# Kernel tuning notes

Measured on AMD Instinct MI355X. Metric: run time of the kernel, lower is better.

## Reference

```python
import jax, jax.numpy as jnp
import numpy as np

LN_EPS = 1e-5

def setup_inputs() -> dict:
    key = jax.random.key(0)
    ks = jax.random.split(key, 10)
    N, E, H, V, L, OUT, G = 100000, 600000, 128, 65, 4, 32, 64
    x_tokens = jax.random.randint(ks[0], (N, 2), 0, V, dtype=jnp.int32)
    edge_index = jax.random.randint(ks[1], (2, E), 0, N, dtype=jnp.int32)
    batch = jnp.sort(jax.random.randint(ks[2], (N,), 0, G)).astype(jnp.int64)
    s = 0.05
    key_emb = jax.random.normal(ks[3], (V, H), jnp.float32) * s
    val_emb = jax.random.normal(ks[4], (V, H), jnp.float32) * s
    Ws = jax.random.normal(ks[5], (L, H, H), jnp.float32) * (1.0 / np.sqrt(H))
    bs = jax.random.normal(ks[6], (L, H), jnp.float32) * s
    ln_g = jnp.ones((L, H), jnp.float32)
    ln_b = jnp.zeros((L, H), jnp.float32)
    out_W = jax.random.normal(ks[7], (OUT, H), jnp.float32) * (1.0 / np.sqrt(H))
    return {"x_tokens": x_tokens, "edge_index": edge_index, "batch": batch,
            "key_emb": key_emb, "val_emb": val_emb, "Ws": Ws, "bs": bs,
            "ln_g": ln_g, "ln_b": ln_b, "out_W": out_W}

def _layer_norm(x, g, b):
    mu = jnp.mean(x, axis=-1, keepdims=True)
    var = jnp.mean(jnp.square(x - mu), axis=-1, keepdims=True)
    return (x - mu) * jax.lax.rsqrt(var + LN_EPS) * g + b

def reference(x_tokens, edge_index, batch, key_emb, val_emb, Ws, bs, ln_g, ln_b, out_W):
    N = x_tokens.shape[0]
    L = Ws.shape[0]
    # layer-0: key + value embedding lookup -> [N, H]
    x = key_emb[x_tokens[:, 0]] + val_emb[x_tokens[:, 1]]
    # GCN normalization with self-loops (computed once; edges fixed per layer)
    loop = jnp.arange(N, dtype=edge_index.dtype)
    src = jnp.concatenate([edge_index[0], loop])  # [E+N]
    dst = jnp.concatenate([edge_index[1], loop])
    deg = jax.ops.segment_sum(jnp.ones_like(dst, dtype=x.dtype), dst, num_segments=N)
    dis = jnp.where(deg > 0, jax.lax.rsqrt(jnp.maximum(deg, 1.0)), 0.0)
    norm = (dis[src] * dis[dst])[:, None]  # [E+N, 1]
    for i in range(L):
        xw = x @ Ws[i]  # [N, H]
        agg = jax.ops.segment_sum(norm * xw[src], dst, num_segments=N) + bs[i]
        new_x = jax.nn.relu(agg)          # use_activation
        x = x + new_x                      # use_residual
        x = _layer_norm(x, ln_g[i], ln_b[i])  # use_layer_norm
    logits = x @ out_W.T  # Linear(bias=False) -> [N, out_dim]
    return logits
```

## Files before the change

### kernel.cpp

```cpp
#include <hip/hip_runtime.h>

#define H 128
#define LN_EPS 1e-5f
#define TROW 66

typedef unsigned short u16;
typedef unsigned int u32;
typedef __attribute__((ext_vector_type(8))) short bf16x8;
typedef __attribute__((ext_vector_type(4))) float f32x4;

__device__ __forceinline__ float bflo(u32 u){ return __uint_as_float(u << 16); }
__device__ __forceinline__ float bfhi(u32 u){ return __uint_as_float(u & 0xFFFF0000u); }
__device__ __forceinline__ float bf1(u16 u){ return __uint_as_float(((u32)u) << 16); }
__device__ __forceinline__ u16 f2bu(float f){
  u32 u = __float_as_uint(f);
  return (u16)((u + 0x7FFFu + ((u >> 16) & 1u)) >> 16);
}

__device__ __forceinline__ float ldf(const void* p, int i, bool isbf){
  return isbf ? bf1(reinterpret_cast<const u16*>(p)[i])
              : reinterpret_cast<const float*>(p)[i];
}


__global__ void k_convert(const void* __restrict__ kemb, const void* __restrict__ vemb,
                          const void* __restrict__ Ws,   const void* __restrict__ bs,
                          const void* __restrict__ lng,  const void* __restrict__ lnb,
                          const void* __restrict__ outW,
                          float* __restrict__ kemb_f, float* __restrict__ vemb_f,
                          u16* __restrict__ W_c, float* __restrict__ bs_f,
                          float* __restrict__ lng_f, float* __restrict__ lnb_f,
                          u16* __restrict__ outW_b, int* __restrict__ flag,
                          int V, int L, int OUT){
  bool isbf = (*reinterpret_cast<const u32*>(lng) == 0x3F803F80u);
  if (blockIdx.x == 0 && threadIdx.x == 0) flag[0] = isbf ? 1 : 0;
  int i = blockIdx.x * blockDim.x + threadIdx.x;
  int nEmb = V * H;
  int nW   = L * H * H;
  int nVec = L * H;
  int nOut = OUT * H;
  if (i < nEmb){ kemb_f[i] = ldf(kemb, i, isbf); vemb_f[i] = ldf(vemb, i, isbf); }
  if (i < nW){
    int j = i & 7, lane = (i >> 3) & 63, g = i >> 9;
    int s = g & 3, cg = (g >> 2) & 7, l = g >> 5;
    int k = s * 32 + (lane >> 4) * 8 + j;
    int n = cg * 16 + (lane & 15);
    W_c[i] = f2bu(ldf(Ws, l * H * H + k * H + n, isbf));
  }
  if (i < nVec){ bs_f[i] = ldf(bs, i, isbf); lng_f[i] = ldf(lng, i, isbf);
                 lnb_f[i] = ldf(lnb, i, isbf); }
  if (i < nOut){ outW_b[i] = f2bu(ldf(outW, i, isbf)); }
}


__global__ void k_count(const int* __restrict__ dst, int E, int* __restrict__ deg){
  int i = blockIdx.x * blockDim.x + threadIdx.x;
  if (i < E) atomicAdd(&deg[dst[i]], 1);
}

__device__ __forceinline__ int paddedLen(int d){ return (d + 4) & ~3; }

__global__ void k_bsum(const int* __restrict__ deg, int* __restrict__ bsum, int N){
  __shared__ int sh[256];
  int i = blockIdx.x * 256 + threadIdx.x;
  sh[threadIdx.x] = (i < N) ? paddedLen(deg[i]) : 0;
  __syncthreads();
  for (int off = 128; off > 0; off >>= 1){
    if (threadIdx.x < off) sh[threadIdx.x] += sh[threadIdx.x + off];
    __syncthreads();
  }
  if (threadIdx.x == 0) bsum[blockIdx.x] = sh[0];
}

__global__ void k_bscan(int* __restrict__ bsum, int nb){
  __shared__ int sh[1024];
  int t = threadIdx.x;
  sh[t] = (t < nb) ? bsum[t] : 0;
  __syncthreads();
  for (int off = 1; off < 1024; off <<= 1){
    int add = (t >= off) ? sh[t - off] : 0;
    __syncthreads();
    sh[t] += add;
    __syncthreads();
  }
  if (t < nb) bsum[t] = (t > 0) ? sh[t - 1] : 0;
}

__global__ void k_scan2(const int* __restrict__ deg, const int* __restrict__ bsum,
                        int* __restrict__ row_ptr, float* __restrict__ dis,
                        int* __restrict__ cursor, int2* __restrict__ csr, int N){
  __shared__ int sh[256];
  int i = blockIdx.x * 256 + threadIdx.x;
  int d = (i < N) ? deg[i] : 0;
  int v = (i < N) ? paddedLen(d) : 0;
  sh[threadIdx.x] = v;
  __syncthreads();
  for (int off = 1; off < 256; off <<= 1){
    int add = (threadIdx.x >= off) ? sh[threadIdx.x - off] : 0;
    __syncthreads();
    sh[threadIdx.x] += add;
    __syncthreads();
  }
  int excl = sh[threadIdx.x] - v + bsum[blockIdx.x];
  if (i < N){
    row_ptr[i] = excl;
    float r = rsqrtf((float)(d + 1));
    dis[i] = r;
    cursor[i] = 1;
    csr[excl] = make_int2(i * (H / 2), __float_as_int(r * r));
    for (int p = excl + d + 1; p < excl + v; p++)
      csr[p] = make_int2(0, 0);
  }
  if (i == N - 1) row_ptr[N] = excl + v;
}

__global__ void k_fill(const int* __restrict__ src, const int* __restrict__ dst, int E,
                       const float* __restrict__ dis, const int* __restrict__ row_ptr,
                       int* __restrict__ cursor, int2* __restrict__ csr){
  int i = blockIdx.x * blockDim.x + threadIdx.x;
  if (i >= E) return;
  int s = src[i], d = dst[i];
  int pos = atomicAdd(&cursor[d], 1);
  csr[row_ptr[d] + pos] = make_int2(s * (H / 2), __float_as_int(dis[s] * dis[d]));
}


__global__ __launch_bounds__(256) void k_embed(const int* __restrict__ tok,
                        const float* __restrict__ kemb, const float* __restrict__ vemb,
                        u16* __restrict__ xb, int N){
  int n = blockIdx.x * 4 + (threadIdx.x >> 6);
  if (n >= N) return;
  int h0 = (threadIdx.x & 63) * 2;
  int t0 = tok[n * 2], t1 = tok[n * 2 + 1];
  float2 k2 = *reinterpret_cast<const float2*>(&kemb[t0 * H + h0]);
  float2 v2 = *reinterpret_cast<const float2*>(&vemb[t1 * H + h0]);
  *reinterpret_cast<u32*>(&xb[(size_t)n * H + h0]) =
      (u32)f2bu(k2.x + v2.x) | ((u32)f2bu(k2.y + v2.y) << 16);
}


__global__ __launch_bounds__(256) void k_gemm(const u16* __restrict__ xb,
                                              const u16* __restrict__ Wc,
                                              u16* __restrict__ xw, int npairs){
  int wid = threadIdx.x >> 6, lane = threadIdx.x & 63;
  int sp = wid >> 1;
  int ch = wid & 1;
  int r = lane & 15, kq = lane >> 4;
  bf16x8 wf[4][4];
  #pragma unroll
  for (int c = 0; c < 4; c++)
    #pragma unroll
    for (int s = 0; s < 4; s++)
      wf[c][s] = *reinterpret_cast<const bf16x8*>(
          Wc + (size_t)((((ch * 4 + c) * 4 + s) * 64 + lane) << 3));
  for (int p = blockIdx.x; p < npairs; p += gridDim.x){
    int node0 = (p * 2 + sp) << 4;
    const u16* xrow = xb + (size_t)node0 * H + r * H + kq * 8;
    bf16x8 xf[4];
    #pragma unroll
    for (int s = 0; s < 4; s++)
      xf[s] = *reinterpret_cast<const bf16x8*>(xrow + s * 32);
    f32x4 acc[4] = {{0,0,0,0},{0,0,0,0},{0,0,0,0},{0,0,0,0}};
    #pragma unroll
    for (int s = 0; s < 4; s++)
      #pragma unroll
      for (int c = 0; c < 4; c++)
        acc[c] = __builtin_amdgcn_mfma_f32_16x16x32_bf16(wf[c][s], xf[s], acc[c], 0, 0, 0);
    u16* orow = xw + (size_t)(node0 + r) * H + ch * 64 + kq * 4;
    #pragma unroll
    for (int c = 0; c < 4; c++){
      u32 lo = (u32)f2bu(acc[c][0]) | ((u32)f2bu(acc[c][1]) << 16);
      u32 hi = (u32)f2bu(acc[c][2]) | ((u32)f2bu(acc[c][3]) << 16);
      *reinterpret_cast<uint2*>(orow + c * 16) = make_uint2(lo, hi);
    }
  }
}


__device__ __forceinline__ void gather2(const u32* __restrict__ xw32,
    const int* __restrict__ row_ptr, const int2* __restrict__ csr,
    const float* __restrict__ bias, const float* __restrict__ gamma,
    const float* __restrict__ beta,
    u16* __restrict__ xb, int N, u32* __restrict__ tile, bool writeGlobal){
  int lane = threadIdx.x & 63;
  int w = threadIdx.x >> 6;
  int n0 = blockIdx.x * 16 + 2 * w;
  int h0 = lane * 2;
  if (n0 >= N){
    tile[(2 * w) * TROW + lane] = 0;
    tile[(2 * w + 1) * TROW + lane] = 0;
    return;
  }
  bool two = (n0 + 1 < N);
  const int4* csr4 = reinterpret_cast<const int4*>(csr);
  int rs0 = __builtin_amdgcn_readfirstlane(row_ptr[n0]);
  int rm  = __builtin_amdgcn_readfirstlane(row_ptr[n0 + 1]);
  int re1 = two ? __builtin_amdgcn_readfirstlane(row_ptr[n0 + 2]) : rm;
  int len0 = rm - rs0, len1 = re1 - rm;
  int common = min(len0, len1);
  u32 xv0 = *reinterpret_cast<const u32*>(&xb[(size_t)n0 * H + h0]);
  u32 xv1 = two ? *reinterpret_cast<const u32*>(&xb[(size_t)(n0 + 1) * H + h0]) : 0u;
  float2 b2 = *reinterpret_cast<const float2*>(&bias[h0]);
  float2 g2 = *reinterpret_cast<const float2*>(&gamma[h0]);
  float2 t2 = *reinterpret_cast<const float2*>(&beta[h0]);
  float a00 = 0.f, a01 = 0.f, a10 = 0.f, a11 = 0.f;
#define EDGE(CX, CY, A0, A1) { \
    u32 cx = (u32)__builtin_amdgcn_readfirstlane(CX); \
    float wgt = __uint_as_float((u32)__builtin_amdgcn_readfirstlane(CY)); \
    u32 v = xw32[cx + lane]; \
    A0 = fmaf(wgt, bflo(v), A0); A1 = fmaf(wgt, bfhi(v), A1); }
  int i = 0;
  for (; i < common; i += 4){
    int4 ca = csr4[(rs0 + i) >> 1], cb = csr4[((rs0 + i) >> 1) + 1];
    int4 da = csr4[(rm + i) >> 1],  db = csr4[((rm + i) >> 1) + 1];
    EDGE(ca.x, ca.y, a00, a01) EDGE(da.x, da.y, a10, a11)
    EDGE(ca.z, ca.w, a00, a01) EDGE(da.z, da.w, a10, a11)
    EDGE(cb.x, cb.y, a00, a01) EDGE(db.x, db.y, a10, a11)
    EDGE(cb.z, cb.w, a00, a01) EDGE(db.z, db.w, a10, a11)
  }
  for (; i < len0; i += 4){
    int4 ca = csr4[(rs0 + i) >> 1], cb = csr4[((rs0 + i) >> 1) + 1];
    EDGE(ca.x, ca.y, a00, a01) EDGE(ca.z, ca.w, a00, a01)
    EDGE(cb.x, cb.y, a00, a01) EDGE(cb.z, cb.w, a00, a01)
  }
  for (; i < len1; i += 4){
    int4 da = csr4[(rm + i) >> 1], db = csr4[((rm + i) >> 1) + 1];
    EDGE(da.x, da.y, a10, a11) EDGE(da.z, da.w, a10, a11)
    EDGE(db.x, db.y, a10, a11) EDGE(db.z, db.w, a10, a11)
  }
#undef EDGE
  float v0 = fmaxf(a00 + b2.x, 0.f), v1 = fmaxf(a01 + b2.y, 0.f);
  v0 += bflo(xv0); v1 += bfhi(xv0);
  float u0 = fmaxf(a10 + b2.x, 0.f), u1 = fmaxf(a11 + b2.y, 0.f);
  u0 += bflo(xv1); u1 += bfhi(xv1);
  float s0 = v0 + v1, s1 = u0 + u1;
  #pragma unroll
  for (int off = 32; off > 0; off >>= 1){
    s0 += __shfl_xor(s0, off);
    s1 += __shfl_xor(s1, off);
  }
  float mu0 = s0 * (1.f / 128.f), mu1 = s1 * (1.f / 128.f);
  float d00 = v0 - mu0, d01 = v1 - mu0;
  float d10 = u0 - mu1, d11 = u1 - mu1;
  float q0 = d00 * d00 + d01 * d01, q1 = d10 * d10 + d11 * d11;
  #pragma unroll
  for (int off = 32; off > 0; off >>= 1){
    q0 += __shfl_xor(q0, off);
    q1 += __shfl_xor(q1, off);
  }
  float inv0 = rsqrtf(q0 * (1.f / 128.f) + LN_EPS);
  float inv1 = rsqrtf(q1 * (1.f / 128.f) + LN_EPS);
  u32 w0 = (u32)f2bu(d00 * inv0 * g2.x + t2.x) |
           ((u32)f2bu(d01 * inv0 * g2.y + t2.y) << 16);
  u32 w1 = (u32)f2bu(d10 * inv1 * g2.x + t2.x) |
           ((u32)f2bu(d11 * inv1 * g2.y + t2.y) << 16);
  tile[(2 * w) * TROW + lane] = w0;
  tile[(2 * w + 1) * TROW + lane] = two ? w1 : 0u;
  if (writeGlobal){
    *reinterpret_cast<u32*>(&xb[(size_t)n0 * H + h0]) = w0;
    if (two)
      *reinterpret_cast<u32*>(&xb[(size_t)(n0 + 1) * H + h0]) = w1;
  }
}

__global__ __launch_bounds__(512) void k_fgemm(const u32* __restrict__ xw32,
    const int* __restrict__ row_ptr, const int2* __restrict__ csr,
    const float* __restrict__ bias, const float* __restrict__ gamma,
    const float* __restrict__ beta,
    u16* __restrict__ xb, const u16* __restrict__ Wc,
    u16* __restrict__ xw_out, int N){
  __shared__ u32 tile[16 * TROW];
  int lane = threadIdx.x & 63, w = threadIdx.x >> 6;
  int r = lane & 15, kq = lane >> 4;
  bf16x8 wfr[4];
  #pragma unroll
  for (int s = 0; s < 4; s++)
    wfr[s] = *reinterpret_cast<const bf16x8*>(Wc + (size_t)(((w * 4 + s) * 64 + lane) << 3));
  gather2(xw32, row_ptr, csr, bias, gamma, beta, xb, N, tile, true);
  __syncthreads();
  int node = blockIdx.x * 16 + r;
  if (node >= N) return;
  const u16* t16 = reinterpret_cast<const u16*>(tile);
  f32x4 acc = {0.f, 0.f, 0.f, 0.f};
  #pragma unroll
  for (int s = 0; s < 4; s++){
    bf16x8 xf = *reinterpret_cast<const bf16x8*>(t16 + r * (2 * TROW) + s * 32 + kq * 8);
    acc = __builtin_amdgcn_mfma_f32_16x16x32_bf16(wfr[s], xf, acc, 0, 0, 0);
  }
  u32 lo = (u32)f2bu(acc[0]) | ((u32)f2bu(acc[1]) << 16);
  u32 hi = (u32)f2bu(acc[2]) | ((u32)f2bu(acc[3]) << 16);
  *reinterpret_cast<uint2*>(xw_out + (size_t)node * H + w * 16 + kq * 4) =
      make_uint2(lo, hi);
}

__global__ __launch_bounds__(512) void k_fout(const u32* __restrict__ xw32,
    const int* __restrict__ row_ptr, const int2* __restrict__ csr,
    const float* __restrict__ bias, const float* __restrict__ gamma,
    const float* __restrict__ beta,
    u16* __restrict__ xb, const u16* __restrict__ oWb,
    u16* __restrict__ out16, float* __restrict__ outf,
    const int* __restrict__ flag, int N){
  __shared__ u32 tile[16 * TROW];
  int lane = threadIdx.x & 63, w = threadIdx.x >> 6;
  int r = lane & 15, kq = lane >> 4;
  bf16x8 wfr[4];
  if (w < 2){
    #pragma unroll
    for (int s = 0; s < 4; s++)
      wfr[s] = *reinterpret_cast<const bf16x8*>(oWb + (w * 16 + r) * H + s * 32 + kq * 8);
  }
  gather2(xw32, row_ptr, csr, bias, gamma, beta, xb, N, tile, false);
  __syncthreads();
  if (w >= 2) return;
  int node = blockIdx.x * 16 + r;
  if (node >= N) return;
  const u16* t16 = reinterpret_cast<const u16*>(tile);
  f32x4 acc = {0.f, 0.f, 0.f, 0.f};
  #pragma unroll
  for (int s = 0; s < 4; s++){
    bf16x8 xf = *reinterpret_cast<const bf16x8*>(t16 + r * (2 * TROW) + s * 32 + kq * 8);
    acc = __builtin_amdgcn_mfma_f32_16x16x32_bf16(wfr[s], xf, acc, 0, 0, 0);
  }
  if (flag[0]){
    u32 lo = (u32)f2bu(acc[0]) | ((u32)f2bu(acc[1]) << 16);
    u32 hi = (u32)f2bu(acc[2]) | ((u32)f2bu(acc[3]) << 16);
    *reinterpret_cast<uint2*>(out16 + (size_t)node * 32 + w * 16 + kq * 4) =
        make_uint2(lo, hi);
  } else {
    *reinterpret_cast<f32x4*>(outf + (size_t)node * 32 + w * 16 + kq * 4) = acc;
  }
}


extern "C" void kernel_launch(void* const* d_in, const int* in_sizes, int n_in,
                              void* d_out, int out_size, void* d_ws, size_t ws_size,
                              hipStream_t stream){
  const int*  x_tokens = (const int*)d_in[0];
  const int*  edge_idx = (const int*)d_in[1];
  const void* kemb = d_in[3];
  const void* vemb = d_in[4];
  const void* Ws   = d_in[5];
  const void* bs   = d_in[6];
  const void* lng  = d_in[7];
  const void* lnb  = d_in[8];
  const void* outW = d_in[9];

  int N   = in_sizes[0] / 2;
  int E   = in_sizes[1] / 2;
  int V   = in_sizes[3] / H;
  int L   = in_sizes[5] / (H * H);
  int OUT = in_sizes[9] / H;

  char* ws = (char*)d_ws;
  size_t off = 0;
  auto alloc = [&](size_t bytes) -> void* {
    void* p = ws + off;
    off += (bytes + 255) & ~(size_t)255;
    return p;
  };
  u16*   xb     = (u16*)  alloc((size_t)N * H * 2);
  u16*   xwA    = (u16*)  alloc((size_t)N * H * 2);
  u16*   xwB    = (u16*)  alloc((size_t)N * H * 2);
  int*   deg    = (int*)  alloc((size_t)N * 4);
  int*   cursor = (int*)  alloc((size_t)N * 4);
  int*   row_ptr= (int*)  alloc((size_t)(N + 1) * 4);
  float* dis    = (float*)alloc((size_t)N * 4);
  int*   bsum   = (int*)  alloc(1024 * 4);
  int2*  csr    = (int2*) alloc(((size_t)E + 4 * (size_t)N) * 8);
  float* kemb_f = (float*)alloc((size_t)V * H * 4);
  float* vemb_f = (float*)alloc((size_t)V * H * 4);
  u16*   W_c    = (u16*)  alloc((size_t)L * H * H * 2);
  float* bs_f   = (float*)alloc((size_t)L * H * 4);
  float* lng_f  = (float*)alloc((size_t)L * H * 4);
  float* lnb_f  = (float*)alloc((size_t)L * H * 4);
  u16*   outW_b = (u16*)  alloc((size_t)OUT * H * 2);
  int*   flag   = (int*)  alloc(256);

  const int* esrc = edge_idx;
  const int* edst = edge_idx + E;

  (void)hipMemsetAsync(deg, 0, (size_t)N * 4, stream);

  int convTotal = L * H * H;
  int cb = (convTotal + 255) / 256;
  k_convert<<<cb, 256, 0, stream>>>(kemb, vemb, Ws, bs, lng, lnb, outW,
                                    kemb_f, vemb_f, W_c, bs_f, lng_f, lnb_f,
                                    outW_b, flag, V, L, OUT);

  int eb = (E + 255) / 256;
  int nb = (N + 255) / 256;
  k_count<<<eb, 256, 0, stream>>>(edst, E, deg);
  k_bsum <<<nb, 256, 0, stream>>>(deg, bsum, N);
  k_bscan<<<1, 1024, 0, stream>>>(bsum, nb);
  k_scan2<<<nb, 256, 0, stream>>>(deg, bsum, row_ptr, dis, cursor, csr, N);
  k_fill <<<eb, 256, 0, stream>>>(esrc, edst, E, dis, row_ptr, cursor, csr);
  k_embed<<<(N + 3) / 4, 256, 0, stream>>>(x_tokens, kemb_f, vemb_f, xb, N);

  int nstrips = (N + 15) / 16;
  int npairs  = (nstrips + 1) / 2;
  k_gemm<<<1024, 256, 0, stream>>>(xb, W_c, xwA, npairs);
  u16* xw_in = xwA; u16* xw_out = xwB;
  for (int l = 0; l < L - 1; l++){
    k_fgemm<<<nstrips, 512, 0, stream>>>((const u32*)xw_in, row_ptr, csr,
                                         bs_f + l * H, lng_f + l * H, lnb_f + l * H,
                                         xb, W_c + (size_t)(l + 1) * H * H,
                                         xw_out, N);
    u16* t = xw_in; xw_in = xw_out; xw_out = t;
  }
  k_fout<<<nstrips, 512, 0, stream>>>((const u32*)xw_in, row_ptr, csr,
                                      bs_f + (L - 1) * H, lng_f + (L - 1) * H,
                                      lnb_f + (L - 1) * H,
                                      xb, outW_b, (u16*)d_out, (float*)d_out,
                                      flag, N);
}
```

Baseline: 297.2 us.

## Gather four nodes per wavefront and halve block size in fused layers

```diff
diff --git a/kernel.cpp b/kernel.cpp
--- a/kernel.cpp
+++ b/kernel.cpp
@@ -177,93 +177,136 @@
 }
 
 
-__device__ __forceinline__ void gather2(const u32* __restrict__ xw32,
+__device__ __forceinline__ void gather4(const u32* __restrict__ xw32,
     const int* __restrict__ row_ptr, const int2* __restrict__ csr,
     const float* __restrict__ bias, const float* __restrict__ gamma,
     const float* __restrict__ beta,
     u16* __restrict__ xb, int N, u32* __restrict__ tile, bool writeGlobal){
   int lane = threadIdx.x & 63;
   int w = threadIdx.x >> 6;
-  int n0 = blockIdx.x * 16 + 2 * w;
+  int n0 = blockIdx.x * 16 + 4 * w;
   int h0 = lane * 2;
-  if (n0 >= N){
-    tile[(2 * w) * TROW + lane] = 0;
-    tile[(2 * w + 1) * TROW + lane] = 0;
-    return;
-  }
-  bool two = (n0 + 1 < N);
   const int4* csr4 = reinterpret_cast<const int4*>(csr);
-  int rs0 = __builtin_amdgcn_readfirstlane(row_ptr[n0]);
-  int rm  = __builtin_amdgcn_readfirstlane(row_ptr[n0 + 1]);
-  int re1 = two ? __builtin_amdgcn_readfirstlane(row_ptr[n0 + 2]) : rm;
-  int len0 = rm - rs0, len1 = re1 - rm;
-  int common = min(len0, len1);
-  u32 xv0 = *reinterpret_cast<const u32*>(&xb[(size_t)n0 * H + h0]);
-  u32 xv1 = two ? *reinterpret_cast<const u32*>(&xb[(size_t)(n0 + 1) * H + h0]) : 0u;
+  int rp0 = __builtin_amdgcn_readfirstlane(row_ptr[min(n0, N)]);
+  int rp1 = __builtin_amdgcn_readfirstlane(row_ptr[min(n0 + 1, N)]);
+  int rp2 = __builtin_amdgcn_readfirstlane(row_ptr[min(n0 + 2, N)]);
+  int rp3 = __builtin_amdgcn_readfirstlane(row_ptr[min(n0 + 3, N)]);
+  int rp4 = __builtin_amdgcn_readfirstlane(row_ptr[min(n0 + 4, N)]);
+  int l0 = rp1 - rp0, l1 = rp2 - rp1, l2 = rp3 - rp2, l3 = rp4 - rp3;
+  bool val0 = n0 < N, val1 = n0 + 1 < N, val2 = n0 + 2 < N, val3 = n0 + 3 < N;
+  u32 xv0 = val0 ? *reinterpret_cast<const u32*>(&xb[(size_t)n0 * H + h0]) : 0u;
+  u32 xv1 = val1 ? *reinterpret_cast<const u32*>(&xb[(size_t)(n0 + 1) * H + h0]) : 0u;
+  u32 xv2 = val2 ? *reinterpret_cast<const u32*>(&xb[(size_t)(n0 + 2) * H + h0]) : 0u;
+  u32 xv3 = val3 ? *reinterpret_cast<const u32*>(&xb[(size_t)(n0 + 3) * H + h0]) : 0u;
   float2 b2 = *reinterpret_cast<const float2*>(&bias[h0]);
   float2 g2 = *reinterpret_cast<const float2*>(&gamma[h0]);
   float2 t2 = *reinterpret_cast<const float2*>(&beta[h0]);
   float a00 = 0.f, a01 = 0.f, a10 = 0.f, a11 = 0.f;
+  float a20 = 0.f, a21 = 0.f, a30 = 0.f, a31 = 0.f;
 #define EDGE(CX, CY, A0, A1) { \
     u32 cx = (u32)__builtin_amdgcn_readfirstlane(CX); \
     float wgt = __uint_as_float((u32)__builtin_amdgcn_readfirstlane(CY)); \
     u32 v = xw32[cx + lane]; \
     A0 = fmaf(wgt, bflo(v), A0); A1 = fmaf(wgt, bfhi(v), A1); }
+  int c01 = min(l0, l1), c23 = min(l2, l3), c4 = min(c01, c23);
   int i = 0;
-  for (; i < common; i += 4){
-    int4 ca = csr4[(rs0 + i) >> 1], cb = csr4[((rs0 + i) >> 1) + 1];
-    int4 da = csr4[(rm + i) >> 1],  db = csr4[((rm + i) >> 1) + 1];
-    EDGE(ca.x, ca.y, a00, a01) EDGE(da.x, da.y, a10, a11)
-    EDGE(ca.z, ca.w, a00, a01) EDGE(da.z, da.w, a10, a11)
-    EDGE(cb.x, cb.y, a00, a01) EDGE(db.x, db.y, a10, a11)
-    EDGE(cb.z, cb.w, a00, a01) EDGE(db.z, db.w, a10, a11)
-  }
-  for (; i < len0; i += 4){
-    int4 ca = csr4[(rs0 + i) >> 1], cb = csr4[((rs0 + i) >> 1) + 1];
-    EDGE(ca.x, ca.y, a00, a01) EDGE(ca.z, ca.w, a00, a01)
-    EDGE(cb.x, cb.y, a00, a01) EDGE(cb.z, cb.w, a00, a01)
-  }
-  for (; i < len1; i += 4){
-    int4 da = csr4[(rm + i) >> 1], db = csr4[((rm + i) >> 1) + 1];
-    EDGE(da.x, da.y, a10, a11) EDGE(da.z, da.w, a10, a11)
-    EDGE(db.x, db.y, a10, a11) EDGE(db.z, db.w, a10, a11)
+  for (; i < c4; i += 4){
+    int4 A0 = csr4[(rp0 + i) >> 1], B0 = csr4[((rp0 + i) >> 1) + 1];
+    int4 A1 = csr4[(rp1 + i) >> 1], B1 = csr4[((rp1 + i) >> 1) + 1];
+    int4 A2 = csr4[(rp2 + i) >> 1], B2 = csr4[((rp2 + i) >> 1) + 1];
+    int4 A3 = csr4[(rp3 + i) >> 1], B3 = csr4[((rp3 + i) >> 1) + 1];
+    EDGE(A0.x, A0.y, a00, a01) EDGE(A1.x, A1.y, a10, a11)
+    EDGE(A2.x, A2.y, a20, a21) EDGE(A3.x, A3.y, a30, a31)
+    EDGE(A0.z, A0.w, a00, a01) EDGE(A1.z, A1.w, a10, a11)
+    EDGE(A2.z, A2.w, a20, a21) EDGE(A3.z, A3.w, a30, a31)
+    EDGE(B0.x, B0.y, a00, a01) EDGE(B1.x, B1.y, a10, a11)
+    EDGE(B2.x, B2.y, a20, a21) EDGE(B3.x, B3.y, a30, a31)
+    EDGE(B0.z, B0.w, a00, a01) EDGE(B1.z, B1.w, a10, a11)
+    EDGE(B2.z, B2.w, a20, a21) EDGE(B3.z, B3.w, a30, a31)
+  }
+  int j = i;
+  for (; j < c01; j += 4){
+    int4 A0 = csr4[(rp0 + j) >> 1], B0 = csr4[((rp0 + j) >> 1) + 1];
+    int4 A1 = csr4[(rp1 + j) >> 1], B1 = csr4[((rp1 + j) >> 1) + 1];
+    EDGE(A0.x, A0.y, a00, a01) EDGE(A1.x, A1.y, a10, a11)
+    EDGE(A0.z, A0.w, a00, a01) EDGE(A1.z, A1.w, a10, a11)
+    EDGE(B0.x, B0.y, a00, a01) EDGE(B1.x, B1.y, a10, a11)
+    EDGE(B0.z, B0.w, a00, a01) EDGE(B1.z, B1.w, a10, a11)
+  }
+  int j0 = j;
+  for (; j0 < l0; j0 += 4){
+    int4 A0 = csr4[(rp0 + j0) >> 1], B0 = csr4[((rp0 + j0) >> 1) + 1];
+    EDGE(A0.x, A0.y, a00, a01) EDGE(A0.z, A0.w, a00, a01)
+    EDGE(B0.x, B0.y, a00, a01) EDGE(B0.z, B0.w, a00, a01)
+  }
+  int j1 = j;
+  for (; j1 < l1; j1 += 4){
+    int4 A1 = csr4[(rp1 + j1) >> 1], B1 = csr4[((rp1 + j1) >> 1) + 1];
+    EDGE(A1.x, A1.y, a10, a11) EDGE(A1.z, A1.w, a10, a11)
+    EDGE(B1.x, B1.y, a10, a11) EDGE(B1.z, B1.w, a10, a11)
+  }
+  int k = i;
+  for (; k < c23; k += 4){
+    int4 A2 = csr4[(rp2 + k) >> 1], B2 = csr4[((rp2 + k) >> 1) + 1];
+    int4 A3 = csr4[(rp3 + k) >> 1], B3 = csr4[((rp3 + k) >> 1) + 1];
+    EDGE(A2.x, A2.y, a20, a21) EDGE(A3.x, A3.y, a30, a31)
+    EDGE(A2.z, A2.w, a20, a21) EDGE(A3.z, A3.w, a30, a31)
+    EDGE(B2.x, B2.y, a20, a21) EDGE(B3.x, B3.y, a30, a31)
+    EDGE(B2.z, B2.w, a20, a21) EDGE(B3.z, B3.w, a30, a31)
+  }
+  int k2 = k;
+  for (; k2 < l2; k2 += 4){
+    int4 A2 = csr4[(rp2 + k2) >> 1], B2 = csr4[((rp2 + k2) >> 1) + 1];
+    EDGE(A2.x, A2.y, a20, a21) EDGE(A2.z, A2.w, a20, a21)
+    EDGE(B2.x, B2.y, a20, a21) EDGE(B2.z, B2.w, a20, a21)
+  }
+  int k3 = k;
+  for (; k3 < l3; k3 += 4){
+    int4 A3 = csr4[(rp3 + k3) >> 1], B3 = csr4[((rp3 + k3) >> 1) + 1];
+    EDGE(A3.x, A3.y, a30, a31) EDGE(A3.z, A3.w, a30, a31)
+    EDGE(B3.x, B3.y, a30, a31) EDGE(B3.z, B3.w, a30, a31)
   }
 #undef EDGE
-  float v0 = fmaxf(a00 + b2.x, 0.f), v1 = fmaxf(a01 + b2.y, 0.f);
-  v0 += bflo(xv0); v1 += bfhi(xv0);
-  float u0 = fmaxf(a10 + b2.x, 0.f), u1 = fmaxf(a11 + b2.y, 0.f);
-  u0 += bflo(xv1); u1 += bfhi(xv1);
-  float s0 = v0 + v1, s1 = u0 + u1;
+  float v0 = fmaxf(a00 + b2.x, 0.f) + bflo(xv0), v1 = fmaxf(a01 + b2.y, 0.f) + bfhi(xv0);
+  float u0 = fmaxf(a10 + b2.x, 0.f) + bflo(xv1), u1 = fmaxf(a11 + b2.y, 0.f) + bfhi(xv1);
+  float p0 = fmaxf(a20 + b2.x, 0.f) + bflo(xv2), p1 = fmaxf(a21 + b2.y, 0.f) + bfhi(xv2);
+  float r0 = fmaxf(a30 + b2.x, 0.f) + bflo(xv3), r1 = fmaxf(a31 + b2.y, 0.f) + bfhi(xv3);
+  float s0 = v0 + v1, s1 = u0 + u1, s2 = p0 + p1, s3 = r0 + r1;
   #pragma unroll
   for (int off = 32; off > 0; off >>= 1){
-    s0 += __shfl_xor(s0, off);
-    s1 += __shfl_xor(s1, off);
+    s0 += __shfl_xor(s0, off); s1 += __shfl_xor(s1, off);
+    s2 += __shfl_xor(s2, off); s3 += __shfl_xor(s3, off);
   }
   float mu0 = s0 * (1.f / 128.f), mu1 = s1 * (1.f / 128.f);
-  float d00 = v0 - mu0, d01 = v1 - mu0;
-  float d10 = u0 - mu1, d11 = u1 - mu1;
+  float mu2 = s2 * (1.f / 128.f), mu3 = s3 * (1.f / 128.f);
+  float d00 = v0 - mu0, d01 = v1 - mu0, d10 = u0 - mu1, d11 = u1 - mu1;
+  float d20 = p0 - mu2, d21 = p1 - mu2, d30 = r0 - mu3, d31 = r1 - mu3;
   float q0 = d00 * d00 + d01 * d01, q1 = d10 * d10 + d11 * d11;
+  float q2 = d20 * d20 + d21 * d21, q3 = d30 * d30 + d31 * d31;
   #pragma unroll
   for (int off = 32; off > 0; off >>= 1){
-    q0 += __shfl_xor(q0, off);
-    q1 += __shfl_xor(q1, off);
-  }
-  float inv0 = rsqrtf(q0 * (1.f / 128.f) + LN_EPS);
-  float inv1 = rsqrtf(q1 * (1.f / 128.f) + LN_EPS);
-  u32 w0 = (u32)f2bu(d00 * inv0 * g2.x + t2.x) |
-           ((u32)f2bu(d01 * inv0 * g2.y + t2.y) << 16);
-  u32 w1 = (u32)f2bu(d10 * inv1 * g2.x + t2.x) |
-           ((u32)f2bu(d11 * inv1 * g2.y + t2.y) << 16);
-  tile[(2 * w) * TROW + lane] = w0;
-  tile[(2 * w + 1) * TROW + lane] = two ? w1 : 0u;
+    q0 += __shfl_xor(q0, off); q1 += __shfl_xor(q1, off);
+    q2 += __shfl_xor(q2, off); q3 += __shfl_xor(q3, off);
+  }
+  float i0 = rsqrtf(q0 * (1.f / 128.f) + LN_EPS), i1 = rsqrtf(q1 * (1.f / 128.f) + LN_EPS);
+  float i2 = rsqrtf(q2 * (1.f / 128.f) + LN_EPS), i3 = rsqrtf(q3 * (1.f / 128.f) + LN_EPS);
+  u32 w0 = (u32)f2bu(d00 * i0 * g2.x + t2.x) | ((u32)f2bu(d01 * i0 * g2.y + t2.y) << 16);
+  u32 w1 = (u32)f2bu(d10 * i1 * g2.x + t2.x) | ((u32)f2bu(d11 * i1 * g2.y + t2.y) << 16);
+  u32 w2 = (u32)f2bu(d20 * i2 * g2.x + t2.x) | ((u32)f2bu(d21 * i2 * g2.y + t2.y) << 16);
+  u32 w3 = (u32)f2bu(d30 * i3 * g2.x + t2.x) | ((u32)f2bu(d31 * i3 * g2.y + t2.y) << 16);
+  tile[(4 * w + 0) * TROW + lane] = val0 ? w0 : 0u;
+  tile[(4 * w + 1) * TROW + lane] = val1 ? w1 : 0u;
+  tile[(4 * w + 2) * TROW + lane] = val2 ? w2 : 0u;
+  tile[(4 * w + 3) * TROW + lane] = val3 ? w3 : 0u;
   if (writeGlobal){
-    *reinterpret_cast<u32*>(&xb[(size_t)n0 * H + h0]) = w0;
-    if (two)
-      *reinterpret_cast<u32*>(&xb[(size_t)(n0 + 1) * H + h0]) = w1;
-  }
-}
-
-__global__ __launch_bounds__(512) void k_fgemm(const u32* __restrict__ xw32,
+    if (val0) *reinterpret_cast<u32*>(&xb[(size_t)n0 * H + h0]) = w0;
+    if (val1) *reinterpret_cast<u32*>(&xb[(size_t)(n0 + 1) * H + h0]) = w1;
+    if (val2) *reinterpret_cast<u32*>(&xb[(size_t)(n0 + 2) * H + h0]) = w2;
+    if (val3) *reinterpret_cast<u32*>(&xb[(size_t)(n0 + 3) * H + h0]) = w3;
+  }
+}
+
+__global__ __launch_bounds__(256) void k_fgemm(const u32* __restrict__ xw32,
     const int* __restrict__ row_ptr, const int2* __restrict__ csr,
     const float* __restrict__ bias, const float* __restrict__ gamma,
     const float* __restrict__ beta,
@@ -272,28 +315,36 @@
   __shared__ u32 tile[16 * TROW];
   int lane = threadIdx.x & 63, w = threadIdx.x >> 6;
   int r = lane & 15, kq = lane >> 4;
-  bf16x8 wfr[4];
-  #pragma unroll
-  for (int s = 0; s < 4; s++)
-    wfr[s] = *reinterpret_cast<const bf16x8*>(Wc + (size_t)(((w * 4 + s) * 64 + lane) << 3));
-  gather2(xw32, row_ptr, csr, bias, gamma, beta, xb, N, tile, true);
+  bf16x8 wfr[2][4];
+  #pragma unroll
+  for (int c = 0; c < 2; c++)
+    #pragma unroll
+    for (int s = 0; s < 4; s++)
+      wfr[c][s] = *reinterpret_cast<const bf16x8*>(
+          Wc + (size_t)((((2 * w + c) * 4 + s) * 64 + lane) << 3));
+  gather4(xw32, row_ptr, csr, bias, gamma, beta, xb, N, tile, true);
   __syncthreads();
   int node = blockIdx.x * 16 + r;
   if (node >= N) return;
   const u16* t16 = reinterpret_cast<const u16*>(tile);
-  f32x4 acc = {0.f, 0.f, 0.f, 0.f};
+  f32x4 acc[2] = {{0,0,0,0},{0,0,0,0}};
   #pragma unroll
   for (int s = 0; s < 4; s++){
     bf16x8 xf = *reinterpret_cast<const bf16x8*>(t16 + r * (2 * TROW) + s * 32 + kq * 8);
-    acc = __builtin_amdgcn_mfma_f32_16x16x32_bf16(wfr[s], xf, acc, 0, 0, 0);
-  }
-  u32 lo = (u32)f2bu(acc[0]) | ((u32)f2bu(acc[1]) << 16);
-  u32 hi = (u32)f2bu(acc[2]) | ((u32)f2bu(acc[3]) << 16);
-  *reinterpret_cast<uint2*>(xw_out + (size_t)node * H + w * 16 + kq * 4) =
-      make_uint2(lo, hi);
-}
-
-__global__ __launch_bounds__(512) void k_fout(const u32* __restrict__ xw32,
+    #pragma unroll
+    for (int c = 0; c < 2; c++)
+      acc[c] = __builtin_amdgcn_mfma_f32_16x16x32_bf16(wfr[c][s], xf, acc[c], 0, 0, 0);
+  }
+  #pragma unroll
+  for (int c = 0; c < 2; c++){
+    u32 lo = (u32)f2bu(acc[c][0]) | ((u32)f2bu(acc[c][1]) << 16);
+    u32 hi = (u32)f2bu(acc[c][2]) | ((u32)f2bu(acc[c][3]) << 16);
+    *reinterpret_cast<uint2*>(xw_out + (size_t)node * H + (2 * w + c) * 16 + kq * 4) =
+        make_uint2(lo, hi);
+  }
+}
+
+__global__ __launch_bounds__(256) void k_fout(const u32* __restrict__ xw32,
     const int* __restrict__ row_ptr, const int2* __restrict__ csr,
     const float* __restrict__ bias, const float* __restrict__ gamma,
     const float* __restrict__ beta,
@@ -309,7 +360,7 @@
     for (int s = 0; s < 4; s++)
       wfr[s] = *reinterpret_cast<const bf16x8*>(oWb + (w * 16 + r) * H + s * 32 + kq * 8);
   }
-  gather2(xw32, row_ptr, csr, bias, gamma, beta, xb, N, tile, false);
+  gather4(xw32, row_ptr, csr, bias, gamma, beta, xb, N, tile, false);
   __syncthreads();
   if (w >= 2) return;
   int node = blockIdx.x * 16 + r;
@@ -401,13 +452,13 @@
   k_gemm<<<1024, 256, 0, stream>>>(xb, W_c, xwA, npairs);
   u16* xw_in = xwA; u16* xw_out = xwB;
   for (int l = 0; l < L - 1; l++){
-    k_fgemm<<<nstrips, 512, 0, stream>>>((const u32*)xw_in, row_ptr, csr,
+    k_fgemm<<<nstrips, 256, 0, stream>>>((const u32*)xw_in, row_ptr, csr,
                                          bs_f + l * H, lng_f + l * H, lnb_f + l * H,
                                          xb, W_c + (size_t)(l + 1) * H * H,
                                          xw_out, N);
     u16* t = xw_in; xw_in = xw_out; xw_out = t;
   }
-  k_fout<<<nstrips, 512, 0, stream>>>((const u32*)xw_in, row_ptr, csr,
+  k_fout<<<nstrips, 256, 0, stream>>>((const u32*)xw_in, row_ptr, csr,
                                       bs_f + (L - 1) * H, lng_f + (L - 1) * H,
                                       lnb_f + (L - 1) * H,
                                       xb, outW_b, (u16*)d_out, (float*)d_out,
```

After: 284.5 us. 4.3% less time.
